# Kernel tuning notes

Hardware: AMD Instinct MI355X
Metric: run time of the kernel (lower is better)

## Reference

```python
import jax, jax.numpy as jnp
import numpy as np

N = 50000       # nodes
E = 800000      # edges (avg degree 16)
B = 1000        # graphs
PER = 50        # nodes per graph
MUL0, MUL1, MUL2 = 64, 32, 16
NUM_RADIAL = 10
R_MAX = 5.0
NUM_BASIS = 128
NLAYERS = 4
HID = MUL0 + 3 * MUL1 + 5 * MUL2  # 240
DEG_NORM = float(np.sqrt(E / N))   # sqrt(avg degree) = 4.0


def _sph(vec, r):
    # component-normalized real spherical harmonics up to l=2 on unit vectors
    u = vec / (r[:, None] + 1e-9)
    x, y, z = u[:, 0], u[:, 1], u[:, 2]
    c3, c15, c5 = jnp.sqrt(3.0), jnp.sqrt(15.0), jnp.sqrt(5.0)
    return jnp.stack([
        jnp.ones_like(x),                 # l=0
        c3 * x, c3 * y, c3 * z,           # l=1
        c15 * x * y, c15 * y * z,
        0.5 * c5 * (3.0 * z * z - 1.0),
        c15 * x * z,
        0.5 * c15 * (x * x - y * y),      # l=2
    ], axis=1)  # [E, 9]


def setup_inputs() -> dict:
    key = jax.random.key(0)
    ks = jax.random.split(key, 20)
    def nrm(k, shape, fan):
        return jax.random.normal(k, shape, jnp.float32) / np.sqrt(fan)
    inp = {}
    inp['z'] = jax.random.randint(ks[0], (N,), 0, 100)
    inp['pos'] = jax.random.normal(ks[1], (N, 3), jnp.float32) * 2.0
    inp['edge_index'] = jax.random.randint(ks[2], (2, E), 0, N)
    inp['edge_shift'] = jnp.zeros((E, 3), jnp.float32)
    inp['batch'] = jnp.repeat(jnp.arange(B), PER)
    inp['absorber_mask'] = (jnp.arange(N) % PER == 0)  # one absorber per graph
    inp['emb'] = nrm(ks[3], (100, MUL0), 1)
    inp['rw1'] = nrm(ks[4], (NLAYERS, NUM_RADIAL, 64), NUM_RADIAL)
    inp['rb1'] = jnp.zeros((NLAYERS, 64), jnp.float32)
    inp['rw2'] = nrm(ks[5], (NLAYERS, 64, MUL0 + MUL1 + MUL2), 64)
    inp['rb2'] = jnp.zeros((NLAYERS, MUL0 + MUL1 + MUL2), jnp.float32)
    inp['wp0'] = nrm(ks[6], (NLAYERS, MUL0, MUL0), MUL0)
    inp['wp1'] = nrm(ks[7], (NLAYERS, MUL0, MUL1), MUL0)
    inp['wp2'] = nrm(ks[8], (NLAYERS, MUL0, MUL2), MUL0)
    inp['s0'] = nrm(ks[9], (NLAYERS, MUL0, MUL0), MUL0)
    inp['s1'] = nrm(ks[10], (NLAYERS, MUL1, MUL1), MUL1)
    inp['s2'] = nrm(ks[11], (NLAYERS, MUL2, MUL2), MUL2)
    inp['wq'] = nrm(ks[12], (MUL0, MUL0), MUL0)
    inp['wk'] = nrm(ks[13], (MUL0, MUL0), MUL0)
    inp['wv'] = nrm(ks[14], (MUL0, MUL0), MUL0)
    inp['m1'] = nrm(ks[15], (2 * MUL0 + MUL1 + MUL2, 128), 176)
    inp['mb1'] = jnp.zeros((128,), jnp.float32)
    inp['m2'] = nrm(ks[16], (128, NUM_BASIS), 128)
    inp['mb2'] = jnp.zeros((NUM_BASIS,), jnp.float32)
    return inp


def _forward(z, pos, edge_index, edge_shift, batch, absorber_mask, emb,
             rw1, rb1, rw2, rb2, wp0, wp1, wp2, s0, s1, s2,
             wq, wk, wv, m1, mb1, m2, mb2):
    src, dst = edge_index[0], edge_index[1]
    vec = pos[dst] - pos[src] + edge_shift          # [E,3]
    r = jnp.linalg.norm(vec, axis=1)                # [E]
    sh = _sph(vec, r)                               # [E,9]
    # gaussian radial basis on linspace(0, r_max, num_radial)
    centers = jnp.linspace(0.0, R_MAX, NUM_RADIAL)
    gamma = R_MAX / (NUM_RADIAL - 1)
    rbas = jnp.exp(-(((r[:, None] - centers) / gamma) ** 2))  # [E,10]

    # embed scalars, pad l=1/l=2 channels with zeros so all layers share structure
    h = jnp.concatenate([emb[z], jnp.zeros((z.shape[0], HID - MUL0), emb.dtype)], axis=1)

    for L in range(NLAYERS):
        s = h[:, :MUL0]
        v = h[:, MUL0:MUL0 + 3 * MUL1].reshape(-1, MUL1, 3)
        t = h[:, MUL0 + 3 * MUL1:].reshape(-1, MUL2, 5)
        # per-edge radial weights via MLP
        rf = jax.nn.silu(rbas @ rw1[L] + rb1[L]) @ rw2[L] + rb2[L]  # [E,112]
        r0 = rf[:, :MUL0]
        r1 = rf[:, MUL0:MUL0 + MUL1]
        r2 = rf[:, MUL0 + MUL1:]
        ss = s[src]  # gather source scalars [E,64]
        m0 = (ss @ wp0[L]) * r0                                           # [E,64]
        mv = ((ss @ wp1[L]) * r1)[:, :, None] * sh[:, None, 1:4]          # [E,32,3]
        mt = ((ss @ wp2[L]) * r2)[:, :, None] * sh[:, None, 4:9]          # [E,16,5]
        a0 = jax.ops.segment_sum(m0, dst, N) / DEG_NORM
        av = jax.ops.segment_sum(mv, dst, N) / DEG_NORM
        at = jax.ops.segment_sum(mt, dst, N) / DEG_NORM
        s_out = jax.nn.silu(s @ s0[L] + a0)
        v_out = jnp.einsum('nmc,mk->nkc', v, s1[L]) + av
        t_out = jnp.einsum('nmc,mk->nkc', t, s2[L]) + at
        h = jnp.concatenate([s_out, v_out.reshape(-1, 3 * MUL1), t_out.reshape(-1, 5 * MUL2)], axis=1)

    # absorber index per graph (exactly one True per graph)
    mask_i = absorber_mask.astype(jnp.int32)
    abs_idx = jax.ops.segment_sum(jnp.arange(N) * mask_i, batch, B)  # [B]
    s_all = h[:, :MUL0]
    v_all = h[:, MUL0:MUL0 + 3 * MUL1].reshape(-1, MUL1, 3)
    t_all = h[:, MUL0 + 3 * MUL1:].reshape(-1, MUL2, 5)
    s_a = s_all[abs_idx]                       # [B,64]
    norm_v = jnp.sum(v_all[abs_idx] ** 2, -1)  # [B,32] invariant norms
    norm_t = jnp.sum(t_all[abs_idx] ** 2, -1)  # [B,16]

    # absorber-query attention pooling over scalar features
    q = s_a @ wq                               # [B,64]
    kk = s_all @ wk
    vv = s_all @ wv
    logits = jnp.sum(kk * q[batch], -1) / jnp.sqrt(jnp.float32(MUL0))  # [N]
    mx = jax.ops.segment_max(logits, batch, B)
    ex = jnp.exp(logits - mx[batch])
    den = jax.ops.segment_sum(ex, batch, B)
    attn = ex / den[batch]
    c = jax.ops.segment_sum(attn[:, None] * vv, batch, B)  # [B,64]

    z_read = jnp.concatenate([s_a, c, norm_v, norm_t], axis=1)  # [B,176]
    return jax.nn.silu(z_read @ m1 + mb1) @ m2 + mb2            # [B,128]


def reference(z, pos, edge_index, edge_shift, batch, absorber_mask, emb,
              rw1, rb1, rw2, rb2, wp0, wp1, wp2, s0, s1, s2,
              wq, wk, wv, m1, mb1, m2, mb2):
    return _forward(z, pos, edge_index, edge_shift, batch, absorber_mask, emb,
                    rw1, rb1, rw2, rb2, wp0, wp1, wp2, s0, s1, s2,
                    wq, wk, wv, m1, mb1, m2, mb2)
```

## Files before the change

### kernel.cpp

```cpp
#include <hip/hip_runtime.h>
#include <hip/hip_bf16.h>
#include <hip/hip_fp16.h>

#define NN 50000
#define NNP 50048
#define EE 800000
#define BB 1000
#define NB 2048
#define RTMAX 10.0f
#define WPB 4

typedef _Float16 half8 __attribute__((ext_vector_type(8)));
typedef float floatx4 __attribute__((ext_vector_type(4)));

__device__ __forceinline__ float silu(float x){ return x / (1.0f + __expf(-x)); }


__global__ __launch_bounds__(256) void prep_w(
    const float* __restrict__ wp0, const float* __restrict__ wp1, const float* __restrict__ wp2,
    float* __restrict__ wpc)
{
    int t = blockIdx.x * 256 + threadIdx.x;
    if (t >= 4*64*112) return;
    int L = t / (64*112); int r = t % (64*112); int k = r / 112; int j = r % 112;
    float w;
    if (j < 64)      w = wp0[L*64*64 + k*64 + j];
    else if (j < 96) w = wp1[L*64*32 + k*32 + (j-64)];
    else             w = wp2[L*64*16 + k*16 + (j-96)];
    wpc[t] = w;
}

__global__ __launch_bounds__(256) void prep_wT(
    const float* __restrict__ s0, const float* __restrict__ s1, const float* __restrict__ s2,
    const float* __restrict__ wpc,
    float* __restrict__ s0Tp, float* __restrict__ s1Tp, float* __restrict__ s2Tp,
    float* __restrict__ wpTp)
{
    int t = blockIdx.x*256 + threadIdx.x;
    if (t < 4*64*72) {
        int L = t / 4608; int r = t % 4608; int j = r / 72; int k = r % 72;
        s0Tp[t] = (k < 64) ? s0[L*4096 + k*64 + j] : 0.0f;
    }
    if (t < 4*32*40) {
        int L = t / 1280; int r = t % 1280; int j = r / 40; int k = r % 40;
        s1Tp[t] = (k < 32) ? s1[L*1024 + k*32 + j] : 0.0f;
    }
    if (t < 4*16*40) {
        int L = t / 640; int r = t % 640; int j = r / 40; int k = r % 40;
        s2Tp[t] = (k < 16) ? s2[L*256 + k*16 + j] : 0.0f;
    }
    if (t < 4*112*72) {
        int L = t / 8064; int r = t % 8064; int m = r / 72; int k = r % 72;
        wpTp[t] = (k < 64) ? wpc[L*7168 + k*112 + m] : 0.0f;
    }
}

__global__ __launch_bounds__(128) void prep_pt(
    const float* __restrict__ emb, const float* __restrict__ wpc, float* __restrict__ pt)
{
    int zz = blockIdx.x; int j = threadIdx.x;
    __shared__ float er[64];
    if (j < 64) er[j] = emb[zz*64 + j];
    __syncthreads();
    if (j >= 112) return;
    float s = 0.0f;
    #pragma unroll
    for (int k = 0; k < 64; k++) s += er[k] * wpc[k*112 + j];
    pt[zz*112 + j] = s;
}

__global__ __launch_bounds__(256) void hist_kernel(const int* __restrict__ ei, int* __restrict__ deg)
{
    int e = blockIdx.x * 256 + threadIdx.x;
    if (e < EE) atomicAdd(&deg[ei[EE + e]], 1);
}

__global__ __launch_bounds__(256) void scan1(const int* __restrict__ deg,
                                             int* __restrict__ start, int* __restrict__ bsum)
{
    __shared__ int buf[256];
    int tid = threadIdx.x;
    int i = blockIdx.x*256 + tid;
    int v = (i < NN) ? deg[i] : 0;
    buf[tid] = v; __syncthreads();
    #pragma unroll
    for (int off = 1; off < 256; off <<= 1) {
        int t = (tid >= off) ? buf[tid-off] : 0;
        __syncthreads(); buf[tid] += t; __syncthreads();
    }
    if (i < NN) start[i] = buf[tid] - v;
    if (tid == 255) bsum[blockIdx.x] = buf[255];
}
__global__ __launch_bounds__(256) void scan2(int* __restrict__ bsum, int nb)
{
    __shared__ int buf[256];
    int tid = threadIdx.x;
    int v = (tid < nb) ? bsum[tid] : 0;
    buf[tid] = v; __syncthreads();
    #pragma unroll
    for (int off = 1; off < 256; off <<= 1) {
        int t = (tid >= off) ? buf[tid-off] : 0;
        __syncthreads(); buf[tid] += t; __syncthreads();
    }
    if (tid < nb) bsum[tid] = buf[tid] - v;
}
__global__ __launch_bounds__(256) void scan3(int* __restrict__ start, const int* __restrict__ bsum,
                                             int* __restrict__ cursor)
{
    int i = blockIdx.x*256 + threadIdx.x;
    if (i < NN) { int v = start[i] + bsum[blockIdx.x]; start[i] = v; cursor[i] = v; }
    if (i == 0) start[NN] = EE;
}

__global__ __launch_bounds__(256) void geom_scatter(
    const float* __restrict__ pos, const int* __restrict__ ei, const float* __restrict__ shift,
    int* __restrict__ cursor, int4* __restrict__ edata)
{
    int e = blockIdx.x * 256 + threadIdx.x;
    if (e >= EE) return;
    int s = ei[e], d = ei[EE + e];
    float vx = pos[d*3+0] - pos[s*3+0] + shift[e*3+0];
    float vy = pos[d*3+1] - pos[s*3+1] + shift[e*3+1];
    float vz = pos[d*3+2] - pos[s*3+2] + shift[e*3+2];
    float r = sqrtf(vx*vx + vy*vy + vz*vz);
    float inv = 1.0f / (r + 1e-9f);
    float x = vx*inv, y = vy*inv, z = vz*inv;
    int p = atomicAdd(&cursor[d], 1);
    __half2 xy = __floats2half2_rn(x, y);
    __half2 z0 = __floats2half2_rn(z, 0.0f);
    int4 rec;
    rec.x = s;
    rec.y = __float_as_int(r);
    rec.z = *(const int*)&xy;
    rec.w = *(const int*)&z0;
    edata[p] = rec;
}

__global__ __launch_bounds__(128) void build_rf(
    const float* __restrict__ rw1, const float* __restrict__ rb1,
    const float* __restrict__ rw2, const float* __restrict__ rb2,
    float* __restrict__ rfall)
{
    int idx = blockIdx.x;
    int L = idx / (NB+1), bin = idx % (NB+1);
    float r = bin * (RTMAX / NB);
    int t = threadIdx.x;
    __shared__ float h1[64];
    if (t < 64) {
        float s = rb1[L*64 + t];
        #pragma unroll
        for (int i = 0; i < 10; i++) { float a = 1.8f*r - (float)i; s += __expf(-a*a) * rw1[L*640 + i*64 + t]; }
        h1[t] = silu(s);
    }
    __syncthreads();
    if (t < 112) {
        float s = rb2[L*112 + t];
        #pragma unroll 8
        for (int k = 0; k < 64; k++) s += h1[k] * rw2[(size_t)L*7168 + k*112 + t];
        rfall[(size_t)idx*112 + t] = s * 0.25f;
    }
}

__global__ __launch_bounds__(256) void pack_tab(
    const float* __restrict__ rfall, uint2* __restrict__ tabpack)
{
    int t = blockIdx.x*256 + threadIdx.x;
    if (t >= 4*NB*64) return;
    int lane = t & 63;
    int rest = t >> 6;
    int L = rest / NB, bin = rest % NB;
    const float* lo = rfall + (size_t)(L*(NB+1) + bin)*112;
    const float* hi = lo + 112;
    float aLo = lo[lane], aHi = hi[lane];
    float bLo = (lane < 48) ? lo[64+lane] : 0.0f;
    float bHi = (lane < 48) ? hi[64+lane] : 0.0f;
    __half2 ha = __floats2half2_rn(aLo, aHi);
    __half2 hb = __floats2half2_rn(bLo, bHi);
    uint2 o;
    o.x = *(const unsigned*)&ha;
    o.y = *(const unsigned*)&hb;
    tabpack[t] = o;
}

__global__ __launch_bounds__(256) void init_h32(
    const int* __restrict__ z, const float* __restrict__ emb, float* __restrict__ hG)
{
    int n = blockIdx.x; int j = threadIdx.x;
    int zz = z[n];
    hG[(size_t)n*256 + j] = (j < 64) ? emb[zz*64 + j] : 0.0f;
}

__global__ __launch_bounds__(64) void init_P(
    const int* __restrict__ z, const float* __restrict__ pt, unsigned* __restrict__ Ppack)
{
    int n = blockIdx.x; int j = threadIdx.x;
    int zz = z[n];
    float a = pt[zz*112 + j];
    float b = (j < 48) ? pt[zz*112 + 64 + j] : 0.0f;
    __half2 hp = __floats2half2_rn(a, b);
    Ppack[(size_t)n*64 + j] = *(const unsigned*)&hp;
}

__global__ __launch_bounds__(256) void agg_kernel(
    const unsigned* __restrict__ Ppack, const int4* __restrict__ edata,
    const int* __restrict__ start, const uint2* __restrict__ tabp,
    float* __restrict__ acc)
{
    int lane = threadIdx.x & 63;
    int wv   = threadIdx.x >> 6;
    int nA = blockIdx.x*(WPB*2) + wv*2;
    int nB = nA + 1;

    __shared__ float ebuf_s[WPB][2][16*12];
    __shared__ float accb_s[WPB][2][240];

    int p0A = start[nA], p1A = start[nA+1];
    int p1B = start[nB+1];
    float aS_A = 0.0f, aS_B = 0.0f;
    float aB_A[5] = {0,0,0,0,0};
    float aB_B[5] = {0,0,0,0,0};
    bool hasB = lane < 48;
    int sbase = (lane < 32) ? 0 : 3;
    int ncomp = (lane < 32) ? 3 : 5;
    const float binscale = (float)NB / RTMAX;
    const float C3 = 1.7320508075688772f, C15 = 3.872983346207417f, C5 = 2.23606797749979f;

    const char* tabc = (const char*)tabp;
    const char* Pc   = (const char*)Ppack;

    int baseA = p0A, baseB = p1A;
    while (baseA < p1A || baseB < p1B) {
        int cntA = p1A - baseA; cntA = cntA < 0 ? 0 : (cntA > 16 ? 16 : cntA);
        int cntB = p1B - baseB; cntB = cntB < 0 ? 0 : (cntB > 16 ? 16 : cntB);
        #pragma unroll
        for (int s = 0; s < 2; s++) {
            int cnt  = s ? cntB : cntA;
            int base = s ? baseB : baseA;
            if (lane < cnt) {
                int4 rec = edata[base + lane];
                float f = fminf(__int_as_float(rec.y) * binscale, (float)NB - 0.5f);
                int b = (int)f;
                float fr = f - (float)b;
                __half2 xy = *(const __half2*)&rec.z;
                __half2 z0 = *(const __half2*)&rec.w;
                float x = __half2float(xy.x), y = __half2float(xy.y), z = __half2float(z0.x);
                float4* v4 = (float4*)(ebuf_s[wv][s] + lane*12);
                v4[0] = make_float4(__int_as_float(b*512), __int_as_float(rec.x*256), fr, 0.0f);
                v4[1] = make_float4(C3*x, C3*y, C3*z, C15*x*y);
                v4[2] = make_float4(C15*y*z, 0.5f*C5*(3.0f*z*z - 1.0f), C15*x*z, 0.5f*C15*(x*x - y*y));
            }
        }
        asm volatile("s_waitcnt lgkmcnt(0)" ::: "memory");
        #pragma unroll
        for (int s = 0; s < 2; s++) {
            int cnt = s ? cntB : cntA;
            const float* eb = ebuf_s[wv][s];
            float aS_l = 0.0f;
            float aB_l[5] = {0,0,0,0,0};
            #pragma unroll 4
            for (int e = 0; e < 16; e++) {
                if (e < cnt) {
                    const float* ep = eb + e*12;
                    int boff = __float_as_int(ep[0]);
                    int poff = __float_as_int(ep[1]);
                    float fr = ep[2];
                    uint2 tt = *(const uint2*)(tabc + boff + lane*8);
                    unsigned pv = *(const unsigned*)(Pc + poff + lane*4);
                    __half2 ha = *(const __half2*)&tt.x;
                    __half2 hp = *(const __half2*)&pv;
                    float alo = __half2float(ha.x), ahi = __half2float(ha.y);
                    float pA  = __half2float(hp.x);
                    aS_l += (alo + (ahi - alo)*fr) * pA;
                    if (hasB) {
                        __half2 hb = *(const __half2*)&tt.y;
                        float blo = __half2float(hb.x), bhi = __half2float(hb.y);
                        float pB  = __half2float(hp.y);
                        float msg = (blo + (bhi - blo)*fr) * pB;
                        #pragma unroll
                        for (int d = 0; d < 5; d++)
                            if (d < ncomp) aB_l[d] += msg * ep[4 + sbase + d];
                    }
                }
            }
            if (s == 0) {
                aS_A += aS_l;
                #pragma unroll
                for (int d = 0; d < 5; d++) aB_A[d] += aB_l[d];
            } else {
                aS_B += aS_l;
                #pragma unroll
                for (int d = 0; d < 5; d++) aB_B[d] += aB_l[d];
            }
        }
        asm volatile("s_waitcnt lgkmcnt(0)" ::: "memory");
        baseA += 16; baseB += 16;
    }

    #pragma unroll
    for (int s = 0; s < 2; s++) {
        float* ab = accb_s[wv][s];
        ab[lane] = s ? aS_B : aS_A;
        const float* aB = s ? aB_B : aB_A;
        if (lane < 32) {
            #pragma unroll
            for (int d = 0; d < 3; d++) ab[64 + 32*d + lane] = aB[d];
        } else if (lane < 48) {
            #pragma unroll
            for (int d = 0; d < 5; d++) ab[160 + 16*d + (lane-32)] = aB[d];
        }
    }
    asm volatile("s_waitcnt lgkmcnt(0)" ::: "memory");
    #pragma unroll
    for (int s = 0; s < 2; s++) {
        float* arow = acc + (size_t)(nA + s)*240;
        const float* ab = accb_s[wv][s];
        #pragma unroll
        for (int c = lane; c < 240; c += 64) arow[c] = ab[c];
    }
}

__global__ __launch_bounds__(256) void update_kernel(
    float* __restrict__ hG, const float* __restrict__ acc,
    const float* __restrict__ s0Tp, const float* __restrict__ s1Tp, const float* __restrict__ s2Tp,
    const float* __restrict__ wpTp, unsigned* __restrict__ Pnext, int hasNext)
{
    __shared__ _Float16 w0[64*72];
    __shared__ _Float16 w1[32*40];
    __shared__ _Float16 w2[16*40];
    __shared__ _Float16 wpl[112*72];
    __shared__ _Float16 sn[64*72];
    __shared__ _Float16 pbuf[64*120];

    int tid = threadIdx.x;
    int lane = tid & 63, wv = tid >> 6;
    int m = lane & 15, quad = lane >> 4;
    int nblk0 = blockIdx.x * 64;
    int n0 = nblk0 + wv*16;

    for (int i = tid; i < 64*72; i += 256) w0[i] = (_Float16)s0Tp[i];
    for (int i = tid; i < 32*40; i += 256) w1[i] = (_Float16)s1Tp[i];
    for (int i = tid; i < 16*40; i += 256) w2[i] = (_Float16)s2Tp[i];
    for (int i = tid; i < 112*72; i += 256) wpl[i] = (_Float16)wpTp[i];
    __syncthreads();

    size_t hrowm = (size_t)(n0 + m)*256;
    size_t arow0 = (size_t)(n0 + quad*4)*240;
    size_t orow0 = (size_t)(n0 + quad*4)*256;

#define LD8(OFF) ({ \
        float4 v0_ = *(const float4*)(hG + (OFF)); \
        float4 v1_ = *(const float4*)(hG + (OFF) + 4); \
        half8 h_; \
        h_[0] = (_Float16)v0_.x; h_[1] = (_Float16)v0_.y; \
        h_[2] = (_Float16)v0_.z; h_[3] = (_Float16)v0_.w; \
        h_[4] = (_Float16)v1_.x; h_[5] = (_Float16)v1_.y; \
        h_[6] = (_Float16)v1_.z; h_[7] = (_Float16)v1_.w; h_; })

    {
        half8 a0 = LD8(hrowm + 0  + quad*8);
        half8 a1 = LD8(hrowm + 32 + quad*8);
        #pragma unroll
        for (int t = 0; t < 4; t++) {
            int cb = 16*t;
            floatx4 c;
            #pragma unroll
            for (int r = 0; r < 4; r++) c[r] = acc[arow0 + (size_t)r*240 + cb + m];
            c = __builtin_amdgcn_mfma_f32_16x16x32_f16(a0, *(const half8*)&w0[(cb+m)*72 + 0  + quad*8], c, 0, 0, 0);
            c = __builtin_amdgcn_mfma_f32_16x16x32_f16(a1, *(const half8*)&w0[(cb+m)*72 + 32 + quad*8], c, 0, 0, 0);
            #pragma unroll
            for (int r = 0; r < 4; r++) {
                float u = silu(c[r]);
                hG[orow0 + (size_t)r*256 + cb + m] = u;
                sn[(wv*16 + quad*4 + r)*72 + cb + m] = (_Float16)u;
            }
        }
    }
    #pragma unroll
    for (int d = 0; d < 3; d++) {
        int kb = 64 + 32*d;
        half8 av = LD8(hrowm + kb + quad*8);
        #pragma unroll
        for (int t = 0; t < 2; t++) {
            int cb = kb + 16*t;
            floatx4 c;
            #pragma unroll
            for (int r = 0; r < 4; r++) c[r] = acc[arow0 + (size_t)r*240 + cb + m];
            c = __builtin_amdgcn_mfma_f32_16x16x32_f16(av, *(const half8*)&w1[(16*t+m)*40 + quad*8], c, 0, 0, 0);
            #pragma unroll
            for (int r = 0; r < 4; r++) hG[orow0 + (size_t)r*256 + cb + m] = c[r];
        }
    }
    #pragma unroll
    for (int e = 0; e < 5; e++) {
        int kb = 160 + 16*e;
        half8 at_ = LD8(hrowm + kb + quad*8);
        floatx4 c;
        #pragma unroll
        for (int r = 0; r < 4; r++) c[r] = acc[arow0 + (size_t)r*240 + kb + m];
        c = __builtin_amdgcn_mfma_f32_16x16x32_f16(at_, *(const half8*)&w2[m*40 + quad*8], c, 0, 0, 0);
        #pragma unroll
        for (int r = 0; r < 4; r++) hG[orow0 + (size_t)r*256 + kb + m] = c[r];
    }

    if (hasNext) {
        asm volatile("s_waitcnt lgkmcnt(0)" ::: "memory");
        half8 p0 = *(const half8*)&sn[(wv*16 + m)*72 + 0  + quad*8];
        half8 p1 = *(const half8*)&sn[(wv*16 + m)*72 + 32 + quad*8];
        #pragma unroll
        for (int t = 0; t < 7; t++) {
            floatx4 c = {0.0f, 0.0f, 0.0f, 0.0f};
            c = __builtin_amdgcn_mfma_f32_16x16x32_f16(p0, *(const half8*)&wpl[(16*t+m)*72 + 0  + quad*8], c, 0, 0, 0);
            c = __builtin_amdgcn_mfma_f32_16x16x32_f16(p1, *(const half8*)&wpl[(16*t+m)*72 + 32 + quad*8], c, 0, 0, 0);
            #pragma unroll
            for (int r = 0; r < 4; r++) pbuf[(wv*16 + quad*4 + r)*120 + 16*t + m] = (_Float16)c[r];
        }
        __syncthreads();
        for (int i = tid; i < 64*64; i += 256) {
            int node = i >> 6, j = i & 63;
            _Float16 aa = pbuf[node*120 + j];
            _Float16 bb = (j < 48) ? pbuf[node*120 + 64 + j] : (_Float16)0.0f;
            unsigned lo = *(const unsigned short*)&aa;
            unsigned hi = *(const unsigned short*)&bb;
            if (nblk0 + node < NN) Pnext[(size_t)(nblk0 + node)*64 + j] = lo | (hi << 16);
        }
    }
#undef LD8
}

__global__ __launch_bounds__(64) void readout_a(
    const float* __restrict__ hG, const float* __restrict__ wq, const float* __restrict__ wk,
    float* __restrict__ kq, float* __restrict__ zr)
{
    int b = blockIdx.x; int j = threadIdx.x;
    int na = 50 * b;
    const float* hr = hG + (size_t)na*256;
    __shared__ float sa[64], qv[64];
    sa[j] = hr[j];
    __syncthreads();
    float q = 0.0f;
    #pragma unroll 8
    for (int k = 0; k < 64; k++) q += sa[k] * wq[k*64 + j];
    qv[j] = q;
    zr[b*176 + j] = sa[j];
    if (j < 32) {
        float nv = 0.0f;
        #pragma unroll
        for (int c = 0; c < 3; c++) { float v = hr[64 + 32*c + j]; nv += v*v; }
        zr[b*176 + 128 + j] = nv;
    }
    if (j < 16) {
        float nt = 0.0f;
        #pragma unroll
        for (int c = 0; c < 5; c++) { float v = hr[160 + 16*c + j]; nt += v*v; }
        zr[b*176 + 160 + j] = nt;
    }
    __syncthreads();
    float s = 0.0f;
    #pragma unroll 8
    for (int jj = 0; jj < 64; jj++) s += wk[j*64 + jj] * qv[jj];
    kq[b*64 + j] = s;
}

__global__ __launch_bounds__(64) void readout_b(
    const float* __restrict__ hG, const float* __restrict__ kq, const float* __restrict__ wv,
    float* __restrict__ zr)
{
    int b = blockIdx.x; int lane = threadIdx.x;
    __shared__ float hblk[64][51];
    __shared__ float at[64], hbar[64];
    if (lane < 50) {
        const float* hr = hG + (size_t)(50*b + lane)*256;
        #pragma unroll 8
        for (int k = 0; k < 64; k++) hblk[k][lane] = hr[k];
    }
    __syncthreads();
    const float* kqb = kq + b*64;
    float logit = -1e30f;
    if (lane < 50) {
        float t = 0.0f;
        #pragma unroll 8
        for (int k = 0; k < 64; k++) t += hblk[k][lane] * kqb[k];
        logit = t * 0.125f;
    }
    float mx = logit;
    for (int o = 32; o; o >>= 1) mx = fmaxf(mx, __shfl_xor(mx, o));
    float ex = (lane < 50) ? __expf(logit - mx) : 0.0f;
    float den = ex;
    for (int o = 32; o; o >>= 1) den += __shfl_xor(den, o);
    at[lane] = ex / den;
    __syncthreads();
    float hb = 0.0f;
    #pragma unroll 1
    for (int i = 0; i < 50; i++) hb += at[i] * hblk[lane][i];
    hbar[lane] = hb;
    __syncthreads();
    float c = 0.0f;
    #pragma unroll 8
    for (int k = 0; k < 64; k++) c += hbar[k] * wv[k*64 + lane];
    zr[b*176 + 64 + lane] = c;
}

__global__ __launch_bounds__(128) void readout_c(
    const float* __restrict__ zr, const float* __restrict__ m1, const float* __restrict__ mb1,
    const float* __restrict__ m2, const float* __restrict__ mb2, float* __restrict__ out)
{
    int b = blockIdx.x; int j = threadIdx.x;
    __shared__ float z[176], tb[128];
    for (int t = j; t < 176; t += 128) z[t] = zr[b*176 + t];
    __syncthreads();
    float a = mb1[j];
    #pragma unroll 8
    for (int k = 0; k < 176; k++) a += z[k] * m1[k*128 + j];
    tb[j] = silu(a);
    __syncthreads();
    float o = mb2[j];
    #pragma unroll 8
    for (int k = 0; k < 128; k++) o += tb[k] * m2[k*128 + j];
    out[b*128 + j] = o;
}

extern "C" void kernel_launch(void* const* d_in, const int* in_sizes, int n_in,
                              void* d_out, int out_size, void* d_ws, size_t ws_size,
                              hipStream_t stream)
{
    const int*   z     = (const int*)  d_in[0];
    const float* pos   = (const float*)d_in[1];
    const int*   ei    = (const int*)  d_in[2];
    const float* shift = (const float*)d_in[3];
    const float* emb = (const float*)d_in[6];
    const float* rw1 = (const float*)d_in[7];
    const float* rb1 = (const float*)d_in[8];
    const float* rw2 = (const float*)d_in[9];
    const float* rb2 = (const float*)d_in[10];
    const float* wp0 = (const float*)d_in[11];
    const float* wp1 = (const float*)d_in[12];
    const float* wp2 = (const float*)d_in[13];
    const float* s0  = (const float*)d_in[14];
    const float* s1  = (const float*)d_in[15];
    const float* s2  = (const float*)d_in[16];
    const float* wq  = (const float*)d_in[17];
    const float* wk  = (const float*)d_in[18];
    const float* wv  = (const float*)d_in[19];
    const float* m1  = (const float*)d_in[20];
    const float* mb1 = (const float*)d_in[21];
    const float* m2  = (const float*)d_in[22];
    const float* mb2 = (const float*)d_in[23];

    float* ws = (float*)d_ws;
    size_t off = 0;
    int4*  edata = (int4*)(ws + off); off += (size_t)4*EE;
    int*   deg    = (int*)(ws + off); off += NN;
    int*   startA = (int*)(ws + off); off += NN + 4;
    int*   cursor = (int*)(ws + off); off += NN;
    int*   bsum   = (int*)(ws + off); off += 256;
    float* hG  = ws + off; off += (size_t)NNP*256;
    float* acc = ws + off; off += (size_t)NNP*240;
    unsigned* Pa = (unsigned*)(ws + off); off += (size_t)NNP*64;
    unsigned* Pb = (unsigned*)(ws + off); off += (size_t)NNP*64;
    uint2* tabpack = (uint2*)(ws + off); off += (size_t)4*NB*64*2;
    float* wpc = ws + off; off += 4*64*112;
    float* pt  = ws + off; off += 100*112;
    float* s0Tp = ws + off; off += 4*4608;
    float* s1Tp = ws + off; off += 4*1280;
    float* s2Tp = ws + off; off += 4*640;
    float* wpTp = ws + off; off += 4*8064;
    float* kq  = ws + off; off += BB*64;
    float* zr  = ws + off; off += BB*176;
    float* rfall = acc;

    prep_w<<<(4*64*112 + 255)/256, 256, 0, stream>>>(wp0, wp1, wp2, wpc);
    prep_wT<<<(4*8064 + 255)/256, 256, 0, stream>>>(s0, s1, s2, wpc, s0Tp, s1Tp, s2Tp, wpTp);
    prep_pt<<<100, 128, 0, stream>>>(emb, wpc, pt);

    hipMemsetAsync(deg, 0, NN*sizeof(int), stream);
    hist_kernel<<<(EE + 255)/256, 256, 0, stream>>>(ei, deg);
    const int NSB = (NN + 255)/256;
    scan1<<<NSB, 256, 0, stream>>>(deg, startA, bsum);
    scan2<<<1, 256, 0, stream>>>(bsum, NSB);
    scan3<<<NSB, 256, 0, stream>>>(startA, bsum, cursor);
    geom_scatter<<<(EE + 255)/256, 256, 0, stream>>>(pos, ei, shift, cursor, edata);

    build_rf<<<4*(NB+1), 128, 0, stream>>>(rw1, rb1, rw2, rb2, rfall);
    pack_tab<<<(4*NB*64 + 255)/256, 256, 0, stream>>>(rfall, tabpack);
    init_h32<<<NN, 256, 0, stream>>>(z, emb, hG);
    init_P<<<NN, 64, 0, stream>>>(z, pt, Pa);

    unsigned* Pcur = Pa; unsigned* Pnxt = Pb;
    for (int L = 0; L < 4; L++) {
        int hasNext = (L < 3) ? 1 : 0;
        agg_kernel<<<NN/(WPB*2), 256, 0, stream>>>(
            Pcur, edata, startA, tabpack + (size_t)L*NB*64, acc);
        update_kernel<<<NNP/64, 256, 0, stream>>>(
            hG, acc, s0Tp + L*4608, s1Tp + L*1280, s2Tp + L*640,
            wpTp + (hasNext ? (L+1)*8064 : 0), Pnxt, hasNext);
        unsigned* tmp = Pcur; Pcur = Pnxt; Pnxt = tmp;
    }

    readout_a<<<BB, 64, 0, stream>>>(hG, wq, wk, kq, zr);
    readout_b<<<BB, 64, 0, stream>>>(hG, kq, wv, zr);
    readout_c<<<BB, 128, 0, stream>>>(zr, m1, mb1, m2, mb2, (float*)d_out);
}
```

Measured before the change: 788.7 us.

## Fuse prep and init kernels, store table deltas, vectorize edge LDS reads

Merges the three weight-prep kernels and the degree memset into two kernels, fuses init_h32 with init_P, and fuses readout_a with readout_b, cutting several launches and one intermediate buffer. The radial table now stores the low value and the high-minus-low delta, so the aggregation loop saves a subtraction per edge. The per-edge shared-memory record is reordered so metadata comes in as one float4 and each lane reads its spherical-harmonic components as one float4, replacing the predicated per-component loop. Storing the delta in fp16 slightly changes rounding.

Result: faster. 763.7 us, median of 2 (-3.2%).

```diff
diff --git a/kernel.cpp b/kernel.cpp
--- a/kernel.cpp
+++ b/kernel.cpp
@@ -16,27 +16,22 @@
 __device__ __forceinline__ float silu(float x){ return x / (1.0f + __expf(-x)); }
 
 
-__global__ __launch_bounds__(256) void prep_w(
+__global__ __launch_bounds__(256) void prep_a(
     const float* __restrict__ wp0, const float* __restrict__ wp1, const float* __restrict__ wp2,
-    float* __restrict__ wpc)
+    const float* __restrict__ s0, const float* __restrict__ s1, const float* __restrict__ s2,
+    float* __restrict__ wpc, float* __restrict__ s0Tp, float* __restrict__ s1Tp,
+    float* __restrict__ s2Tp, int* __restrict__ deg)
 {
     int t = blockIdx.x * 256 + threadIdx.x;
-    if (t >= 4*64*112) return;
-    int L = t / (64*112); int r = t % (64*112); int k = r / 112; int j = r % 112;
-    float w;
-    if (j < 64)      w = wp0[L*64*64 + k*64 + j];
-    else if (j < 96) w = wp1[L*64*32 + k*32 + (j-64)];
-    else             w = wp2[L*64*16 + k*16 + (j-96)];
-    wpc[t] = w;
-}
-
-__global__ __launch_bounds__(256) void prep_wT(
-    const float* __restrict__ s0, const float* __restrict__ s1, const float* __restrict__ s2,
-    const float* __restrict__ wpc,
-    float* __restrict__ s0Tp, float* __restrict__ s1Tp, float* __restrict__ s2Tp,
-    float* __restrict__ wpTp)
-{
-    int t = blockIdx.x*256 + threadIdx.x;
+    if (t < NN) deg[t] = 0;
+    if (t < 4*64*112) {
+        int L = t / (64*112); int r = t % (64*112); int k = r / 112; int j = r % 112;
+        float w;
+        if (j < 64)      w = wp0[L*64*64 + k*64 + j];
+        else if (j < 96) w = wp1[L*64*32 + k*32 + (j-64)];
+        else             w = wp2[L*64*16 + k*16 + (j-96)];
+        wpc[t] = w;
+    }
     if (t < 4*64*72) {
         int L = t / 4608; int r = t % 4608; int j = r / 72; int k = r % 72;
         s0Tp[t] = (k < 64) ? s0[L*4096 + k*64 + j] : 0.0f;
@@ -49,24 +44,24 @@
         int L = t / 640; int r = t % 640; int j = r / 40; int k = r % 40;
         s2Tp[t] = (k < 16) ? s2[L*256 + k*16 + j] : 0.0f;
     }
+}
+
+__global__ __launch_bounds__(256) void prep_b(
+    const float* __restrict__ wpc, const float* __restrict__ emb,
+    float* __restrict__ wpTp, float* __restrict__ pt)
+{
+    int t = blockIdx.x*256 + threadIdx.x;
     if (t < 4*112*72) {
         int L = t / 8064; int r = t % 8064; int m = r / 72; int k = r % 72;
         wpTp[t] = (k < 64) ? wpc[L*7168 + k*112 + m] : 0.0f;
     }
-}
-
-__global__ __launch_bounds__(128) void prep_pt(
-    const float* __restrict__ emb, const float* __restrict__ wpc, float* __restrict__ pt)
-{
-    int zz = blockIdx.x; int j = threadIdx.x;
-    __shared__ float er[64];
-    if (j < 64) er[j] = emb[zz*64 + j];
-    __syncthreads();
-    if (j >= 112) return;
-    float s = 0.0f;
-    #pragma unroll
-    for (int k = 0; k < 64; k++) s += er[k] * wpc[k*112 + j];
-    pt[zz*112 + j] = s;
+    if (t < 100*112) {
+        int zz = t / 112, j = t % 112;
+        float s = 0.0f;
+        #pragma unroll 8
+        for (int k = 0; k < 64; k++) s += emb[zz*64 + k] * wpc[k*112 + j];
+        pt[t] = s;
+    }
 }
 
 __global__ __launch_bounds__(256) void hist_kernel(const int* __restrict__ ei, int* __restrict__ deg)
@@ -174,31 +169,27 @@
     float aLo = lo[lane], aHi = hi[lane];
     float bLo = (lane < 48) ? lo[64+lane] : 0.0f;
     float bHi = (lane < 48) ? hi[64+lane] : 0.0f;
-    __half2 ha = __floats2half2_rn(aLo, aHi);
-    __half2 hb = __floats2half2_rn(bLo, bHi);
+    __half2 ha = __floats2half2_rn(aLo, aHi - aLo);
+    __half2 hb = __floats2half2_rn(bLo, bHi - bLo);
     uint2 o;
     o.x = *(const unsigned*)&ha;
     o.y = *(const unsigned*)&hb;
     tabpack[t] = o;
 }
 
-__global__ __launch_bounds__(256) void init_h32(
-    const int* __restrict__ z, const float* __restrict__ emb, float* __restrict__ hG)
+__global__ __launch_bounds__(256) void init_hp32(
+    const int* __restrict__ z, const float* __restrict__ emb,
+    const float* __restrict__ pt, float* __restrict__ hG, unsigned* __restrict__ Ppack)
 {
     int n = blockIdx.x; int j = threadIdx.x;
     int zz = z[n];
     hG[(size_t)n*256 + j] = (j < 64) ? emb[zz*64 + j] : 0.0f;
-}
-
-__global__ __launch_bounds__(64) void init_P(
-    const int* __restrict__ z, const float* __restrict__ pt, unsigned* __restrict__ Ppack)
-{
-    int n = blockIdx.x; int j = threadIdx.x;
-    int zz = z[n];
-    float a = pt[zz*112 + j];
-    float b = (j < 48) ? pt[zz*112 + 64 + j] : 0.0f;
-    __half2 hp = __floats2half2_rn(a, b);
-    Ppack[(size_t)n*64 + j] = *(const unsigned*)&hp;
+    if (j < 64) {
+        float a = pt[zz*112 + j];
+        float b = (j < 48) ? pt[zz*112 + 64 + j] : 0.0f;
+        __half2 hp = __floats2half2_rn(a, b);
+        Ppack[(size_t)n*64 + j] = *(const unsigned*)&hp;
+    }
 }
 
 __global__ __launch_bounds__(256) void agg_kernel(
@@ -220,13 +211,14 @@
     float aB_A[5] = {0,0,0,0,0};
     float aB_B[5] = {0,0,0,0,0};
     bool hasB = lane < 48;
-    int sbase = (lane < 32) ? 0 : 3;
-    int ncomp = (lane < 32) ? 3 : 5;
+    bool isT  = lane >= 32;
+    int shqoff = isT ? 8 : 4;
     const float binscale = (float)NB / RTMAX;
     const float C3 = 1.7320508075688772f, C15 = 3.872983346207417f, C5 = 2.23606797749979f;
 
     const char* tabc = (const char*)tabp;
     const char* Pc   = (const char*)Ppack;
+    int lane8 = lane*8, lane4 = lane*4;
 
     int baseA = p0A, baseB = p1A;
     while (baseA < p1A || baseB < p1B) {
@@ -245,9 +237,10 @@
                 __half2 z0 = *(const __half2*)&rec.w;
                 float x = __half2float(xy.x), y = __half2float(xy.y), z = __half2float(z0.x);
                 float4* v4 = (float4*)(ebuf_s[wv][s] + lane*12);
-                v4[0] = make_float4(__int_as_float(b*512), __int_as_float(rec.x*256), fr, 0.0f);
-                v4[1] = make_float4(C3*x, C3*y, C3*z, C15*x*y);
-                v4[2] = make_float4(C15*y*z, 0.5f*C5*(3.0f*z*z - 1.0f), C15*x*z, 0.5f*C15*(x*x - y*y));
+                v4[0] = make_float4(__int_as_float(b*512), __int_as_float(rec.x*256), fr,
+                                    0.5f*C15*(x*x - y*y));
+                v4[1] = make_float4(C3*x, C3*y, C3*z, 0.0f);
+                v4[2] = make_float4(C15*x*y, C15*y*z, 0.5f*C5*(3.0f*z*z - 1.0f), C15*x*z);
             }
         }
         asm volatile("s_waitcnt lgkmcnt(0)" ::: "memory");
@@ -261,24 +254,25 @@
             for (int e = 0; e < 16; e++) {
                 if (e < cnt) {
                     const float* ep = eb + e*12;
-                    int boff = __float_as_int(ep[0]);
-                    int poff = __float_as_int(ep[1]);
-                    float fr = ep[2];
-                    uint2 tt = *(const uint2*)(tabc + boff + lane*8);
-                    unsigned pv = *(const unsigned*)(Pc + poff + lane*4);
+                    float4 md = *(const float4*)ep;
+                    int boff = __float_as_int(md.x);
+                    int poff = __float_as_int(md.y);
+                    float fr = md.z;
+                    uint2 tt = *(const uint2*)(tabc + boff + lane8);
+                    unsigned pv = *(const unsigned*)(Pc + poff + lane4);
                     __half2 ha = *(const __half2*)&tt.x;
                     __half2 hp = *(const __half2*)&pv;
-                    float alo = __half2float(ha.x), ahi = __half2float(ha.y);
-                    float pA  = __half2float(hp.x);
-                    aS_l += (alo + (ahi - alo)*fr) * pA;
+                    float rfA = __half2float(ha.x) + __half2float(ha.y)*fr;
+                    aS_l += rfA * __half2float(hp.x);
                     if (hasB) {
+                        float4 sq = *(const float4*)(ep + shqoff);
                         __half2 hb = *(const __half2*)&tt.y;
-                        float blo = __half2float(hb.x), bhi = __half2float(hb.y);
-                        float pB  = __half2float(hp.y);
-                        float msg = (blo + (bhi - blo)*fr) * pB;
-                        #pragma unroll
-                        for (int d = 0; d < 5; d++)
-                            if (d < ncomp) aB_l[d] += msg * ep[4 + sbase + d];
+                        float rfB = __half2float(hb.x) + __half2float(hb.y)*fr;
+                        float msg = rfB * __half2float(hp.y);
+                        aB_l[0] += msg * sq.x;
+                        aB_l[1] += msg * sq.y;
+                        aB_l[2] += msg * sq.z;
+                        if (isT) { aB_l[3] += msg * sq.w; aB_l[4] += msg * md.w; }
                     }
                 }
             }
@@ -427,15 +421,22 @@
 #undef LD8
 }
 
-__global__ __launch_bounds__(64) void readout_a(
+__global__ __launch_bounds__(64) void readout_ab(
     const float* __restrict__ hG, const float* __restrict__ wq, const float* __restrict__ wk,
-    float* __restrict__ kq, float* __restrict__ zr)
+    const float* __restrict__ wv, float* __restrict__ zr)
 {
     int b = blockIdx.x; int j = threadIdx.x;
     int na = 50 * b;
     const float* hr = hG + (size_t)na*256;
-    __shared__ float sa[64], qv[64];
+    __shared__ float sa[64], qv[64], kqv[64];
+    __shared__ float hblk[64][51];
+    __shared__ float at[64], hbar[64];
     sa[j] = hr[j];
+    if (j < 50) {
+        const float* hrr = hG + (size_t)(50*b + j)*256;
+        #pragma unroll 8
+        for (int k = 0; k < 64; k++) hblk[k][j] = hrr[k];
+    }
     __syncthreads();
     float q = 0.0f;
     #pragma unroll 8
@@ -458,46 +459,31 @@
     float s = 0.0f;
     #pragma unroll 8
     for (int jj = 0; jj < 64; jj++) s += wk[j*64 + jj] * qv[jj];
-    kq[b*64 + j] = s;
-}
-
-__global__ __launch_bounds__(64) void readout_b(
-    const float* __restrict__ hG, const float* __restrict__ kq, const float* __restrict__ wv,
-    float* __restrict__ zr)
-{
-    int b = blockIdx.x; int lane = threadIdx.x;
-    __shared__ float hblk[64][51];
-    __shared__ float at[64], hbar[64];
-    if (lane < 50) {
-        const float* hr = hG + (size_t)(50*b + lane)*256;
-        #pragma unroll 8
-        for (int k = 0; k < 64; k++) hblk[k][lane] = hr[k];
-    }
-    __syncthreads();
-    const float* kqb = kq + b*64;
+    kqv[j] = s;
+    __syncthreads();
     float logit = -1e30f;
-    if (lane < 50) {
+    if (j < 50) {
         float t = 0.0f;
         #pragma unroll 8
-        for (int k = 0; k < 64; k++) t += hblk[k][lane] * kqb[k];
+        for (int k = 0; k < 64; k++) t += hblk[k][j] * kqv[k];
         logit = t * 0.125f;
     }
     float mx = logit;
     for (int o = 32; o; o >>= 1) mx = fmaxf(mx, __shfl_xor(mx, o));
-    float ex = (lane < 50) ? __expf(logit - mx) : 0.0f;
+    float ex = (j < 50) ? __expf(logit - mx) : 0.0f;
     float den = ex;
     for (int o = 32; o; o >>= 1) den += __shfl_xor(den, o);
-    at[lane] = ex / den;
+    at[j] = ex / den;
     __syncthreads();
     float hb = 0.0f;
     #pragma unroll 1
-    for (int i = 0; i < 50; i++) hb += at[i] * hblk[lane][i];
-    hbar[lane] = hb;
+    for (int i = 0; i < 50; i++) hb += at[i] * hblk[j][i];
+    hbar[j] = hb;
     __syncthreads();
     float c = 0.0f;
     #pragma unroll 8
-    for (int k = 0; k < 64; k++) c += hbar[k] * wv[k*64 + lane];
-    zr[b*176 + 64 + lane] = c;
+    for (int k = 0; k < 64; k++) c += hbar[k] * wv[k*64 + j];
+    zr[b*176 + 64 + j] = c;
 }
 
 __global__ __launch_bounds__(128) void readout_c(
@@ -564,15 +550,13 @@
     float* s1Tp = ws + off; off += 4*1280;
     float* s2Tp = ws + off; off += 4*640;
     float* wpTp = ws + off; off += 4*8064;
-    float* kq  = ws + off; off += BB*64;
     float* zr  = ws + off; off += BB*176;
     float* rfall = acc;
 
-    prep_w<<<(4*64*112 + 255)/256, 256, 0, stream>>>(wp0, wp1, wp2, wpc);
-    prep_wT<<<(4*8064 + 255)/256, 256, 0, stream>>>(s0, s1, s2, wpc, s0Tp, s1Tp, s2Tp, wpTp);
-    prep_pt<<<100, 128, 0, stream>>>(emb, wpc, pt);
-
-    hipMemsetAsync(deg, 0, NN*sizeof(int), stream);
+    prep_a<<<(NN + 255)/256, 256, 0, stream>>>(wp0, wp1, wp2, s0, s1, s2,
+                                               wpc, s0Tp, s1Tp, s2Tp, deg);
+    prep_b<<<(4*8064 + 255)/256, 256, 0, stream>>>(wpc, emb, wpTp, pt);
+
     hist_kernel<<<(EE + 255)/256, 256, 0, stream>>>(ei, deg);
     const int NSB = (NN + 255)/256;
     scan1<<<NSB, 256, 0, stream>>>(deg, startA, bsum);
@@ -582,8 +566,7 @@
 
     build_rf<<<4*(NB+1), 128, 0, stream>>>(rw1, rb1, rw2, rb2, rfall);
     pack_tab<<<(4*NB*64 + 255)/256, 256, 0, stream>>>(rfall, tabpack);
-    init_h32<<<NN, 256, 0, stream>>>(z, emb, hG);
-    init_P<<<NN, 64, 0, stream>>>(z, pt, Pa);
+    init_hp32<<<NN, 256, 0, stream>>>(z, emb, pt, hG, Pa);
 
     unsigned* Pcur = Pa; unsigned* Pnxt = Pb;
     for (int L = 0; L < 4; L++) {
@@ -596,7 +579,6 @@
         unsigned* tmp = Pcur; Pcur = Pnxt; Pnxt = tmp;
     }
 
-    readout_a<<<BB, 64, 0, stream>>>(hG, wq, wk, kq, zr);
-    readout_b<<<BB, 64, 0, stream>>>(hG, kq, wv, zr);
+    readout_ab<<<BB, 64, 0, stream>>>(hG, wq, wk, wv, zr);
     readout_c<<<BB, 128, 0, stream>>>(zr, m1, mb1, m2, mb2, (float*)d_out);
 }
```
